# Kernel tuning notes

Hardware: AMD Instinct MI355X
Metric: run time of the kernel (lower is better)

## Reference

```python
import jax, jax.numpy as jnp
import numpy as np

DT = 0.1  # source sets dt = 0.1 globally
B, XS, SS, H = 128, 64, 16, 512  # batch, x_size, s_size, hidden_size


def setup_inputs() -> dict:
    key = jax.random.key(0)
    ks = jax.random.split(key, 14)
    sc = 1.0 / np.sqrt(H)  # PyTorch LSTM/Linear init bound
    u = lambda k, shape: jax.random.uniform(k, shape, jnp.float32, -sc, sc)
    return {
        "x": jax.random.normal(ks[0], (B, XS), jnp.float32),
        "s0": jax.random.normal(ks[1], (B, SS), jnp.float32),
        # LSTM layer 0 (input = x_size + s_size), gate order i,f,g,o
        "W_ih0": u(ks[2], (4 * H, XS + SS)),
        "W_hh0": u(ks[3], (4 * H, H)),
        "b_ih0": u(ks[4], (4 * H,)),
        "b_hh0": u(ks[5], (4 * H,)),
        # LSTM layer 1 (input = hidden)
        "W_ih1": u(ks[6], (4 * H, H)),
        "W_hh1": u(ks[7], (4 * H, H)),
        "b_ih1": u(ks[8], (4 * H,)),
        "b_hh1": u(ks[9], (4 * H,)),
        # fc: hidden -> s_size
        "W_fc": u(ks[10], (SS, H)),
        "b_fc": u(ks[11], (SS,)),
        "max_time": 20,
    }


def _lstm_cell(h, c, inp, W_ih, W_hh, b_ih, b_hh):
    g = inp @ W_ih.T + b_ih + h @ W_hh.T + b_hh  # [B, 4H]
    i, f, gg, o = jnp.split(g, 4, axis=-1)  # torch gate order i,f,g,o
    c = jax.nn.sigmoid(f) * c + jax.nn.sigmoid(i) * jnp.tanh(gg)
    h = jax.nn.sigmoid(o) * jnp.tanh(c)
    return h, c


def reference(x, s0, W_ih0, W_hh0, b_ih0, b_hh0, W_ih1, W_hh1, b_ih1, b_hh1, W_fc, b_fc, max_time):
    T = int(max_time / DT) + 1  # while cal_t <= max_time, cal_t += dt
    batch = x.shape[0]
    hid = W_hh0.shape[1]
    zeros = jnp.zeros((batch, hid), x.dtype)
    init = (zeros, zeros, zeros, zeros, s0)  # (h0,c0,h1,c1,current_s)

    def step(carry, _):
        h0, c0, h1, c1, s = carry
        inp = jnp.concatenate([x, s], axis=-1)  # [B, XS+SS]
        h0, c0 = _lstm_cell(h0, c0, inp, W_ih0, W_hh0, b_ih0, b_hh0)
        h1, c1 = _lstm_cell(h1, c1, h0, W_ih1, W_hh1, b_ih1, b_hh1)
        step_out = h1 @ W_fc.T + b_fc  # [B, SS] (dropout is identity in eval)
        s = s + step_out * DT  # residual Euler update
        return (h0, c0, h1, c1, s), (s, step_out)

    _, (outs, res) = jax.lax.scan(step, init, None, length=T)
    outputs = jnp.transpose(outs, (1, 0, 2))  # [B, T, SS]
    res_steps = jnp.transpose(res, (1, 0, 2))  # [B, T, SS]
    cal_times = jnp.arange(T, dtype=x.dtype) * DT
    return outputs, cal_times, res_steps
```

## Files before the change

### kernel.cpp

```cpp
#include <hip/hip_runtime.h>

#define NB    256
#define BT    1024
#define BATCH 128
#define HID   512
#define XSZ   64
#define SSZ   16
#define CPAD  32
#define SPIN_MAX (1 << 17)

typedef unsigned int uint;
typedef unsigned long long ulong64;
typedef _Float16 half2v __attribute__((ext_vector_type(2)));

#define AL8(p)    __hip_atomic_load((const ulong64*)(p), __ATOMIC_RELAXED, __HIP_MEMORY_SCOPE_AGENT)
#define AS4(p, v) __hip_atomic_store((uint*)(p), (v), __ATOMIC_RELAXED, __HIP_MEMORY_SCOPE_AGENT)

__device__ __align__(16) uint4 g_h0Q[2][64 * 128];
__device__ __align__(16) uint4 g_h1Q[2][64 * 128];
__device__ __align__(16) float g_Wcomb[4 * HID * HID];
__device__ int g_cnt[512 * 8 * CPAD];

__device__ __forceinline__ float sigf(float x) { return 1.f / (1.f + __expf(-x)); }
__device__ __forceinline__ float tanh_fast(float x) {
  float ax = fabsf(x); float e = __expf(-2.f * ax);
  return copysignf((1.f - e) / (1.f + e), x);
}
__device__ __forceinline__ uint pack_f16(float a, float b) {
  half2v h; h.x = (_Float16)a; h.y = (_Float16)b;
  return __builtin_bit_cast(uint, h);
}
__device__ __forceinline__ float2 up2(uint u) {
  half2v h = __builtin_bit_cast(half2v, u);
  return make_float2((float)h.x, (float)h.y);
}
__device__ __forceinline__ float fdot2(uint a, uint w, float c) {
#if __has_builtin(__builtin_amdgcn_fdot2)
  return __builtin_amdgcn_fdot2(__builtin_bit_cast(half2v, a),
                                __builtin_bit_cast(half2v, w), c, false);
#else
  float2 av = up2(a), wv = up2(w);
  return fmaf(av.x, wv.x, fmaf(av.y, wv.y, c));
#endif
}
__device__ __forceinline__ void dot8(uint a, uint4 w0, uint4 w1, float* acc) {
  acc[0] = fdot2(a, w0.x, acc[0]); acc[1] = fdot2(a, w0.y, acc[1]);
  acc[2] = fdot2(a, w0.z, acc[2]); acc[3] = fdot2(a, w0.w, acc[3]);
  acc[4] = fdot2(a, w1.x, acc[4]); acc[5] = fdot2(a, w1.y, acc[5]);
  acc[6] = fdot2(a, w1.z, acc[6]); acc[7] = fdot2(a, w1.w, acc[7]);
}
__device__ __forceinline__ void dots16x2(const uint4* __restrict__ apq,
                                         const uint*  __restrict__ wbA,
                                         const uint*  __restrict__ wbB,
                                         float* __restrict__ accA,
                                         float* __restrict__ accB) {
  const ulong64* ap = (const ulong64*)apq;
  ulong64 lo[16], hi[16];
#pragma unroll
  for (int i = 0; i < 16; ++i) {
    lo[i] = AL8(ap + i * 256);
    hi[i] = AL8(ap + i * 256 + 1);
  }
#pragma unroll
  for (int i = 0; i < 16; ++i) {
    const uint4* wA = (const uint4*)(wbA + 32 * i);
    const uint4* wB = (const uint4*)(wbB + 32 * i);
    uint a0 = (uint)lo[i], a1 = (uint)(lo[i] >> 32);
    uint a2 = (uint)hi[i], a3 = (uint)(hi[i] >> 32);
    dot8(a0, wA[0], wA[1], accA); dot8(a0, wB[0], wB[1], accB);
    dot8(a1, wA[2], wA[3], accA); dot8(a1, wB[2], wB[3], accB);
    dot8(a2, wA[4], wA[5], accA); dot8(a2, wB[4], wB[5], accB);
    dot8(a3, wA[6], wA[7], accA); dot8(a3, wB[6], wB[7], accB);
  }
}

__device__ __forceinline__ void cnt_wait(int pid) {
  const int l = threadIdx.x & 63;
  const int* cp = &g_cnt[(pid * 8 + (l & 7)) * CPAD];
  int guard = 0;
  for (;;) {
    int v = __hip_atomic_load(cp, __ATOMIC_RELAXED, __HIP_MEMORY_SCOPE_AGENT);
    if (__all(v >= 64)) break;
    __builtin_amdgcn_s_sleep(1);
    if (++guard > SPIN_MAX) break;
  }
  __builtin_amdgcn_sched_barrier(0);
}

__device__ __forceinline__ void group_wait(int pid, int pw, int tid, int* rel) {
  if ((tid >> 6) == pw) {
    cnt_wait(pid);
    if ((tid & 63) == 0)
      __hip_atomic_store(&rel[pid & 1], pid, __ATOMIC_RELEASE, __HIP_MEMORY_SCOPE_WORKGROUP);
  } else {
    int guard = 0;
    while (__hip_atomic_load(&rel[pid & 1], __ATOMIC_ACQUIRE, __HIP_MEMORY_SCOPE_WORKGROUP) < pid) {
      __builtin_amdgcn_s_sleep(1);
      if (++guard > SPIN_MAX) break;
    }
    __builtin_amdgcn_sched_barrier(0);
  }
}

__global__ void setup_kernel(float* __restrict__ out, int T) {
  int idx = blockIdx.x * blockDim.x + threadIdx.x;
  int n   = gridDim.x * blockDim.x;
  uint* z0 = (uint*)g_h0Q;
  uint* z1 = (uint*)g_h1Q;
  for (int i = idx; i < 2 * 64 * 128 * 4; i += n) { z0[i] = 0u; z1[i] = 0u; }
  for (int t = idx; t < T; t += n) out[BATCH * T * SSZ + t] = (float)t * 0.1f;
  for (int i = idx; i < 512 * 8 * CPAD; i += n) g_cnt[i] = 0;
}

__global__ void wcomb_kernel(const float* __restrict__ Wih0, const float* __restrict__ Wfc) {
  int idx = blockIdx.x * blockDim.x + threadIdx.x;
  int row = idx >> 9, k = idx & (HID - 1);
  float a = 0.f;
#pragma unroll
  for (int m = 0; m < SSZ; m++) a += Wih0[row * (XSZ + SSZ) + XSZ + m] * Wfc[m * HID + k];
  g_Wcomb[idx] = 0.1f * a;
}

__global__ __launch_bounds__(BT, 4) void persist_kernel(
    const float* __restrict__ x,    const float* __restrict__ s0,
    const float* __restrict__ Wih0, const float* __restrict__ Whh0,
    const float* __restrict__ bih0, const float* __restrict__ bhh0,
    const float* __restrict__ Wih1, const float* __restrict__ Whh1,
    const float* __restrict__ bih1, const float* __restrict__ bhh1,
    const float* __restrict__ Wfc,  const float* __restrict__ bfc,
    float* __restrict__ out, int T)
{
  __shared__ uint  lwT[4][256][8];
  __shared__ float gbuf[8][8][128];
  __shared__ float gbuf1[4][8][128];
  __shared__ float sbase[8][128];
  __shared__ float c0s[2][128], c1s[2][128];
  __shared__ uint  wfcP[16][268];
  __shared__ float b1s[8], ucs[8];
  __shared__ int   rel[2];

  const int bk  = blockIdx.x;
  const int tid = threadIdx.x;
  const int ks  = tid >> 7;
  const int b   = tid & 127;
  const int q0  = (ks & 3) * 16;
  const int kp0 = (ks & 3) * 64;

  if (tid == 0) { rel[0] = -1; rel[1] = -1; }

  for (int e = tid; e < 4 * 256 * 8; e += BT) {
    int mat = e >> 11, kp = (e >> 3) & 255, r = e & 7;
    int row = (r >> 1) * HID + 2 * bk + (r & 1);
    const float* src = (mat == 0) ? &Whh0[row * HID]
                     : (mat == 1) ? &g_Wcomb[row * HID]
                     : (mat == 2) ? &Wih1[row * HID] : &Whh1[row * HID];
    lwT[mat][kp][r] = pack_f16(src[2 * kp], src[2 * kp + 1]);
  }
  for (int e = tid; e < 16 * 256; e += BT) {
    int fs_ = e >> 8, kp = e & 255;
    wfcP[fs_][kp] = pack_f16(Wfc[fs_ * HID + 2 * kp], Wfc[fs_ * HID + 2 * kp + 1]);
  }
  for (int e = tid; e < 4 * 8 * 128; e += BT) ((float*)gbuf)[e] = 0.f;
  {
    int r = tid >> 7, bb = tid & 127;
    int row = (r >> 1) * HID + 2 * bk + (r & 1);
    float a = bih0[row] + bhh0[row];
    const float* wr = Wih0 + row * (XSZ + SSZ);
#pragma unroll 4
    for (int k = 0; k < XSZ; k++) a = fmaf(wr[k], x[bb * XSZ + k], a);
    sbase[r][bb] = a;
  }
  if (tid < 8) {
    int row = (tid >> 1) * HID + 2 * bk + (tid & 1);
    b1s[tid] = bih1[row] + bhh1[row];
    float uc = 0.f;
    const float* ws = Wih0 + row * (XSZ + SSZ) + XSZ;
#pragma unroll
    for (int m = 0; m < SSZ; m++) uc = fmaf(ws[m], bfc[m], uc);
    ucs[tid] = 0.1f * uc;
  }
  __syncthreads();

  float u[8];
  if (tid < 128) {
#pragma unroll
    for (int r = 0; r < 8; r++) {
      int row = (r >> 1) * HID + 2 * bk + (r & 1);
      const float* ws = Wih0 + row * (XSZ + SSZ) + XSZ;
      float a = 0.f;
#pragma unroll
      for (int m = 0; m < SSZ; m++) a = fmaf(ws[m], s0[b * SSZ + m], a);
      u[r] = a - ucs[r];
    }
    c0s[0][b] = 0.f; c0s[1][b] = 0.f;
    c1s[0][b] = 0.f; c1s[1][b] = 0.f;
  }

  const bool fcw = (bk >= 128) && ((tid >> 6) == 15);
  const int  fb = bk - 128, lane = tid & 63, fs = lane & 15, fq = lane >> 4;
  float s_reg = 0.f, bfcj = 0.f;
  if (fcw && lane < SSZ) { s_reg = s0[fb * SSZ + lane]; bfcj = bfc[lane]; }

  auto fc_step = [&](int tt, const uint4* h1base) {
    const ulong64* hp = (const ulong64*)(h1base + fq * 16 * 128 + fb);
    ulong64 lo[16], hi[16];
#pragma unroll
    for (int i = 0; i < 16; ++i) {
      lo[i] = AL8(hp + i * 256);
      hi[i] = AL8(hp + i * 256 + 1);
    }
    const uint4* wp = (const uint4*)&wfcP[fs][fq * 64];
    float acc = 0.f;
#pragma unroll
    for (int i = 0; i < 16; ++i) {
      uint4 w = wp[i];
      acc = fdot2((uint)lo[i],         w.x, acc);
      acc = fdot2((uint)(lo[i] >> 32), w.y, acc);
      acc = fdot2((uint)hi[i],         w.z, acc);
      acc = fdot2((uint)(hi[i] >> 32), w.w, acc);
    }
    acc += __shfl_xor(acc, 16);
    acc += __shfl_xor(acc, 32);
    if (lane < SSZ) {
      float so = acc + bfcj;
      s_reg += 0.1f * so;
      out[fb * (T * SSZ) + tt * SSZ + fs] = s_reg;
      out[BATCH * T * SSZ + T + fb * (T * SSZ) + tt * SSZ + fs] = so;
    }
  };

  int p = 0;
  for (int t = 0; t < T; ++t) {
    if (ks >= 4) {
      if (t > 0) group_wait(2 * t, 8, tid, rel);
      float accA[8] = {0,0,0,0,0,0,0,0}, accB[8] = {0,0,0,0,0,0,0,0};
      dots16x2(g_h1Q[p] + q0 * 128 + b, &lwT[1][kp0][0], &lwT[3][kp0][0], accA, accB);
#pragma unroll
      for (int r = 0; r < 8; r++) { gbuf[ks][r][b] = accA[r]; gbuf1[ks - 4][r][b] = accB[r]; }
    }
    __syncthreads();
    if (tid < 128) {
      float pre[8];
#pragma unroll
      for (int r = 0; r < 8; r++) {
        float s1 = gbuf[0][r][b] + gbuf[1][r][b] + gbuf[2][r][b] + gbuf[3][r][b];
        float s2 = gbuf[4][r][b] + gbuf[5][r][b] + gbuf[6][r][b] + gbuf[7][r][b];
        u[r] += s2 + ucs[r];
        pre[r] = sbase[r][b] + s1 + u[r];
      }
      float h[2];
#pragma unroll
      for (int jj = 0; jj < 2; jj++) {
        float c = c0s[jj][b];
        c = sigf(pre[2 + jj]) * c + sigf(pre[0 + jj]) * tanh_fast(pre[4 + jj]);
        c0s[jj][b] = c;
        h[jj] = sigf(pre[6 + jj]) * tanh_fast(c);
      }
      AS4(((uint*)&g_h0Q[p ^ 1][(bk >> 2) * 128 + b]) + (bk & 3), pack_f16(h[0], h[1]));
      asm volatile("s_waitcnt vmcnt(0)" ::: "memory");
      if ((tid & 63) == 0)
        __hip_atomic_fetch_add(&g_cnt[((2 * t + 1) * 8 + (bk & 7)) * CPAD], 1,
                               __ATOMIC_RELAXED, __HIP_MEMORY_SCOPE_AGENT);
    }
    __syncthreads();
    if (ks < 4) {
      group_wait(2 * t + 1, 0, tid, rel);
      float accA[8] = {0,0,0,0,0,0,0,0}, accB[8] = {0,0,0,0,0,0,0,0};
      dots16x2(g_h0Q[p ^ 1] + q0 * 128 + b, &lwT[2][kp0][0], &lwT[0][kp0][0], accA, accB);
#pragma unroll
      for (int r = 0; r < 8; r++) { gbuf[4 + ks][r][b] = accA[r]; gbuf[ks][r][b] = accB[r]; }
    } else {
      if (fcw && t > 0) fc_step(t - 1, g_h1Q[p]);
    }
    __syncthreads();
    if (tid < 128) {
      float pre[8];
#pragma unroll
      for (int r = 0; r < 8; r++) {
        float s1 = gbuf[4][r][b] + gbuf[5][r][b] + gbuf[6][r][b] + gbuf[7][r][b];
        float s2 = gbuf1[0][r][b] + gbuf1[1][r][b] + gbuf1[2][r][b] + gbuf1[3][r][b];
        pre[r] = b1s[r] + s1 + s2;
      }
      float h[2];
#pragma unroll
      for (int jj = 0; jj < 2; jj++) {
        float c = c1s[jj][b];
        c = sigf(pre[2 + jj]) * c + sigf(pre[0 + jj]) * tanh_fast(pre[4 + jj]);
        c1s[jj][b] = c;
        h[jj] = sigf(pre[6 + jj]) * tanh_fast(c);
      }
      AS4(((uint*)&g_h1Q[p ^ 1][(bk >> 2) * 128 + b]) + (bk & 3), pack_f16(h[0], h[1]));
      asm volatile("s_waitcnt vmcnt(0)" ::: "memory");
      if ((tid & 63) == 0)
        __hip_atomic_fetch_add(&g_cnt[((2 * t + 2) * 8 + (bk & 7)) * CPAD], 1,
                               __ATOMIC_RELAXED, __HIP_MEMORY_SCOPE_AGENT);
    }
    __syncthreads();
    p ^= 1;
  }

  if (fcw) {
    cnt_wait(2 * T);
    fc_step(T - 1, g_h1Q[p]);
  }
}

extern "C" void kernel_launch(void* const* d_in, const int* in_sizes, int n_in,
                              void* d_out, int out_size, void* d_ws, size_t ws_size,
                              hipStream_t stream) {
  const float* x    = (const float*)d_in[0];
  const float* s0   = (const float*)d_in[1];
  const float* Wih0 = (const float*)d_in[2];
  const float* Whh0 = (const float*)d_in[3];
  const float* bih0 = (const float*)d_in[4];
  const float* bhh0 = (const float*)d_in[5];
  const float* Wih1 = (const float*)d_in[6];
  const float* Whh1 = (const float*)d_in[7];
  const float* bih1 = (const float*)d_in[8];
  const float* bhh1 = (const float*)d_in[9];
  const float* Wfc  = (const float*)d_in[10];
  const float* bfc  = (const float*)d_in[11];
  float* out = (float*)d_out;

  const int T = out_size / (2 * BATCH * SSZ + 1);

  setup_kernel<<<64, 256, 0, stream>>>(out, T);
  wcomb_kernel<<<(4 * HID * HID) / 256, 256, 0, stream>>>(Wih0, Wfc);
  persist_kernel<<<NB, BT, 0, stream>>>(x, s0, Wih0, Whh0, bih0, bhh0,
                                        Wih1, Whh1, bih1, bhh1, Wfc, bfc, out, T);
}
```

Baseline: 4.849 ms.

## Spread gate nonlinearity across all threads and use per-quarter arrival counters

The cell update now runs across all 1024 threads, one gate row per thread, with shuffles gathering the i/f/g/o values. Before, only 128 threads did this work, and a block-wide barrier stood between the update and the next matmul. Each block now counts its wavefronts' arrivals in shared memory and bumps one of four global counters, one per quarter of the blocks. Each consumer quarter waits only on the counter for the slice of h it reads, instead of on a broader group wait. This aims to cut the serial elementwise tail and the per-step barrier latency, at the cost of shuffle traffic, spin loops on thread 0, and a larger counter array.

```diff
diff --git a/kernel.cpp b/kernel.cpp
--- a/kernel.cpp
+++ b/kernel.cpp
@@ -19,7 +19,7 @@
 __device__ __align__(16) uint4 g_h0Q[2][64 * 128];
 __device__ __align__(16) uint4 g_h1Q[2][64 * 128];
 __device__ __align__(16) float g_Wcomb[4 * HID * HID];
-__device__ int g_cnt[512 * 8 * CPAD];
+__device__ int g_cnt[2100 * 4 * CPAD];
 
 __device__ __forceinline__ float sigf(float x) { return 1.f / (1.f + __expf(-x)); }
 __device__ __forceinline__ float tanh_fast(float x) {
@@ -49,57 +49,42 @@
   acc[4] = fdot2(a, w1.x, acc[4]); acc[5] = fdot2(a, w1.y, acc[5]);
   acc[6] = fdot2(a, w1.z, acc[6]); acc[7] = fdot2(a, w1.w, acc[7]);
 }
-__device__ __forceinline__ void dots16x2(const uint4* __restrict__ apq,
-                                         const uint*  __restrict__ wbA,
-                                         const uint*  __restrict__ wbB,
-                                         float* __restrict__ accA,
-                                         float* __restrict__ accB) {
+__device__ __forceinline__ void dots_dual(const uint4* __restrict__ apq,
+                                          const uint*  __restrict__ wbA,
+                                          const uint*  __restrict__ wbB,
+                                          float* __restrict__ accA,
+                                          float* __restrict__ accB) {
   const ulong64* ap = (const ulong64*)apq;
-  ulong64 lo[16], hi[16];
-#pragma unroll
-  for (int i = 0; i < 16; ++i) {
-    lo[i] = AL8(ap + i * 256);
-    hi[i] = AL8(ap + i * 256 + 1);
-  }
-#pragma unroll
-  for (int i = 0; i < 16; ++i) {
-    const uint4* wA = (const uint4*)(wbA + 32 * i);
-    const uint4* wB = (const uint4*)(wbB + 32 * i);
-    uint a0 = (uint)lo[i], a1 = (uint)(lo[i] >> 32);
-    uint a2 = (uint)hi[i], a3 = (uint)(hi[i] >> 32);
-    dot8(a0, wA[0], wA[1], accA); dot8(a0, wB[0], wB[1], accB);
-    dot8(a1, wA[2], wA[3], accA); dot8(a1, wB[2], wB[3], accB);
-    dot8(a2, wA[4], wA[5], accA); dot8(a2, wB[4], wB[5], accB);
-    dot8(a3, wA[6], wA[7], accA); dot8(a3, wB[6], wB[7], accB);
-  }
-}
-
-__device__ __forceinline__ void cnt_wait(int pid) {
-  const int l = threadIdx.x & 63;
-  const int* cp = &g_cnt[(pid * 8 + (l & 7)) * CPAD];
+#pragma unroll
+  for (int c = 0; c < 2; ++c) {
+    ulong64 lo[8], hi[8];
+#pragma unroll
+    for (int i = 0; i < 8; ++i) {
+      lo[i] = AL8(ap + (c * 8 + i) * 256);
+      hi[i] = AL8(ap + (c * 8 + i) * 256 + 1);
+    }
+#pragma unroll
+    for (int i = 0; i < 8; ++i) {
+      const uint4* wA = (const uint4*)(wbA + 32 * (c * 8 + i));
+      const uint4* wB = (const uint4*)(wbB + 32 * (c * 8 + i));
+      uint a0 = (uint)lo[i], a1 = (uint)(lo[i] >> 32);
+      uint a2 = (uint)hi[i], a3 = (uint)(hi[i] >> 32);
+      dot8(a0, wA[0], wA[1], accA); dot8(a0, wB[0], wB[1], accB);
+      dot8(a1, wA[2], wA[3], accA); dot8(a1, wB[2], wB[3], accB);
+      dot8(a2, wA[4], wA[5], accA); dot8(a2, wB[4], wB[5], accB);
+      dot8(a3, wA[6], wA[7], accA); dot8(a3, wB[6], wB[7], accB);
+    }
+  }
+}
+
+__device__ __forceinline__ void qwait(int pid, int qtr) {
+  const int* cp = &g_cnt[(pid * 4 + qtr) * CPAD];
   int guard = 0;
-  for (;;) {
-    int v = __hip_atomic_load(cp, __ATOMIC_RELAXED, __HIP_MEMORY_SCOPE_AGENT);
-    if (__all(v >= 64)) break;
+  while (__hip_atomic_load(cp, __ATOMIC_RELAXED, __HIP_MEMORY_SCOPE_AGENT) < NB / 4) {
     __builtin_amdgcn_s_sleep(1);
     if (++guard > SPIN_MAX) break;
   }
   __builtin_amdgcn_sched_barrier(0);
-}
-
-__device__ __forceinline__ void group_wait(int pid, int pw, int tid, int* rel) {
-  if ((tid >> 6) == pw) {
-    cnt_wait(pid);
-    if ((tid & 63) == 0)
-      __hip_atomic_store(&rel[pid & 1], pid, __ATOMIC_RELEASE, __HIP_MEMORY_SCOPE_WORKGROUP);
-  } else {
-    int guard = 0;
-    while (__hip_atomic_load(&rel[pid & 1], __ATOMIC_ACQUIRE, __HIP_MEMORY_SCOPE_WORKGROUP) < pid) {
-      __builtin_amdgcn_s_sleep(1);
-      if (++guard > SPIN_MAX) break;
-    }
-    __builtin_amdgcn_sched_barrier(0);
-  }
 }
 
 __global__ void setup_kernel(float* __restrict__ out, int T) {
@@ -109,7 +94,8 @@
   uint* z1 = (uint*)g_h1Q;
   for (int i = idx; i < 2 * 64 * 128 * 4; i += n) { z0[i] = 0u; z1[i] = 0u; }
   for (int t = idx; t < T; t += n) out[BATCH * T * SSZ + t] = (float)t * 0.1f;
-  for (int i = idx; i < 512 * 8 * CPAD; i += n) g_cnt[i] = 0;
+  int ncnt = (2 * T + 2) * 4 * CPAD;
+  for (int i = idx; i < ncnt; i += n) g_cnt[i] = 0;
 }
 
 __global__ void wcomb_kernel(const float* __restrict__ Wih0, const float* __restrict__ Wfc) {
@@ -131,73 +117,61 @@
     float* __restrict__ out, int T)
 {
   __shared__ uint  lwT[4][256][8];
-  __shared__ float gbuf[8][8][128];
-  __shared__ float gbuf1[4][8][128];
-  __shared__ float sbase[8][128];
-  __shared__ float c0s[2][128], c1s[2][128];
+  __shared__ float gA[4][8][130];
+  __shared__ float gW[4][8][130];
+  __shared__ float gB[8][8][130];
   __shared__ uint  wfcP[16][268];
-  __shared__ float b1s[8], ucs[8];
-  __shared__ int   rel[2];
-
-  const int bk  = blockIdx.x;
-  const int tid = threadIdx.x;
-  const int ks  = tid >> 7;
-  const int b   = tid & 127;
-  const int q0  = (ks & 3) * 16;
-  const int kp0 = (ks & 3) * 64;
-
-  if (tid == 0) { rel[0] = -1; rel[1] = -1; }
+  __shared__ int   arrive;
+
+  const int bk   = blockIdx.x;
+  const int tid  = threadIdx.x;
+  const int ks   = tid >> 7;
+  const int bb   = tid & 127;
+  const int wv   = tid >> 6;
+  const int lane = tid & 63;
+  const int be   = (wv << 3) + (lane >> 3);
+  const int r    = lane & 7;
+  const int myq  = bk >> 6;
+
+  if (tid == 0) arrive = 0;
 
   for (int e = tid; e < 4 * 256 * 8; e += BT) {
-    int mat = e >> 11, kp = (e >> 3) & 255, r = e & 7;
-    int row = (r >> 1) * HID + 2 * bk + (r & 1);
+    int mat = e >> 11, kp = (e >> 3) & 255, rr = e & 7;
+    int row = (rr >> 1) * HID + 2 * bk + (rr & 1);
     const float* src = (mat == 0) ? &Whh0[row * HID]
                      : (mat == 1) ? &g_Wcomb[row * HID]
                      : (mat == 2) ? &Wih1[row * HID] : &Whh1[row * HID];
-    lwT[mat][kp][r] = pack_f16(src[2 * kp], src[2 * kp + 1]);
+    lwT[mat][kp][rr] = pack_f16(src[2 * kp], src[2 * kp + 1]);
   }
   for (int e = tid; e < 16 * 256; e += BT) {
     int fs_ = e >> 8, kp = e & 255;
     wfcP[fs_][kp] = pack_f16(Wfc[fs_ * HID + 2 * kp], Wfc[fs_ * HID + 2 * kp + 1]);
   }
-  for (int e = tid; e < 4 * 8 * 128; e += BT) ((float*)gbuf)[e] = 0.f;
+  for (int e = tid; e < 4 * 8 * 130; e += BT) ((float*)gW)[e] = 0.f;
+
+  const int row_g = (r >> 1) * HID + 2 * bk + (r & 1);
+  float sbase_t = bih0[row_g] + bhh0[row_g];
   {
-    int r = tid >> 7, bb = tid & 127;
-    int row = (r >> 1) * HID + 2 * bk + (r & 1);
-    float a = bih0[row] + bhh0[row];
-    const float* wr = Wih0 + row * (XSZ + SSZ);
+    const float* wr = Wih0 + row_g * (XSZ + SSZ);
 #pragma unroll 4
-    for (int k = 0; k < XSZ; k++) a = fmaf(wr[k], x[bb * XSZ + k], a);
-    sbase[r][bb] = a;
-  }
-  if (tid < 8) {
-    int row = (tid >> 1) * HID + 2 * bk + (tid & 1);
-    b1s[tid] = bih1[row] + bhh1[row];
-    float uc = 0.f;
-    const float* ws = Wih0 + row * (XSZ + SSZ) + XSZ;
-#pragma unroll
-    for (int m = 0; m < SSZ; m++) uc = fmaf(ws[m], bfc[m], uc);
-    ucs[tid] = 0.1f * uc;
-  }
-  __syncthreads();
-
-  float u[8];
-  if (tid < 128) {
-#pragma unroll
-    for (int r = 0; r < 8; r++) {
-      int row = (r >> 1) * HID + 2 * bk + (r & 1);
-      const float* ws = Wih0 + row * (XSZ + SSZ) + XSZ;
-      float a = 0.f;
-#pragma unroll
-      for (int m = 0; m < SSZ; m++) a = fmaf(ws[m], s0[b * SSZ + m], a);
-      u[r] = a - ucs[r];
-    }
-    c0s[0][b] = 0.f; c0s[1][b] = 0.f;
-    c1s[0][b] = 0.f; c1s[1][b] = 0.f;
-  }
-
-  const bool fcw = (bk >= 128) && ((tid >> 6) == 15);
-  const int  fb = bk - 128, lane = tid & 63, fs = lane & 15, fq = lane >> 4;
+    for (int k = 0; k < XSZ; k++) sbase_t = fmaf(wr[k], x[be * XSZ + k], sbase_t);
+  }
+  float ucs_t = 0.f, u_t = 0.f;
+  {
+    const float* ws = Wih0 + row_g * (XSZ + SSZ) + XSZ;
+#pragma unroll
+    for (int m = 0; m < SSZ; m++) {
+      ucs_t = fmaf(ws[m], bfc[m], ucs_t);
+      u_t   = fmaf(ws[m], s0[be * SSZ + m], u_t);
+    }
+    ucs_t *= 0.1f;
+    u_t   -= ucs_t;
+  }
+  const float b1_t = bih1[row_g] + bhh1[row_g];
+  float c0_reg = 0.f, c1_reg = 0.f;
+
+  const bool fcw = (bk >= 128) && (wv == 15);
+  const int  fb = bk - 128, fs = lane & 15, fq = lane >> 4;
   float s_reg = 0.f, bfcj = 0.f;
   if (fcw && lane < SSZ) { s_reg = s0[fb * SSZ + lane]; bfcj = bfc[lane]; }
 
@@ -229,78 +203,98 @@
     }
   };
 
-  int p = 0;
+  __syncthreads();
+
+  int p = 0, ph = 0;
   for (int t = 0; t < T; ++t) {
     if (ks >= 4) {
-      if (t > 0) group_wait(2 * t, 8, tid, rel);
+      if (t > 0) qwait(2 * t, ks & 3);
       float accA[8] = {0,0,0,0,0,0,0,0}, accB[8] = {0,0,0,0,0,0,0,0};
-      dots16x2(g_h1Q[p] + q0 * 128 + b, &lwT[1][kp0][0], &lwT[3][kp0][0], accA, accB);
-#pragma unroll
-      for (int r = 0; r < 8; r++) { gbuf[ks][r][b] = accA[r]; gbuf1[ks - 4][r][b] = accB[r]; }
+      dots_dual(g_h1Q[p] + (ks & 3) * 16 * 128 + bb,
+                &lwT[1][(ks & 3) * 64][0], &lwT[3][(ks & 3) * 64][0], accA, accB);
+#pragma unroll
+      for (int r2 = 0; r2 < 8; r2++) { gA[ks - 4][r2][bb] = accA[r2]; gB[ks][r2][bb] = accB[r2]; }
     }
     __syncthreads();
-    if (tid < 128) {
-      float pre[8];
-#pragma unroll
-      for (int r = 0; r < 8; r++) {
-        float s1 = gbuf[0][r][b] + gbuf[1][r][b] + gbuf[2][r][b] + gbuf[3][r][b];
-        float s2 = gbuf[4][r][b] + gbuf[5][r][b] + gbuf[6][r][b] + gbuf[7][r][b];
-        u[r] += s2 + ucs[r];
-        pre[r] = sbase[r][b] + s1 + u[r];
+    {
+      float s1 = gW[0][r][be] + gW[1][r][be] + gW[2][r][be] + gW[3][r][be];
+      float s2 = gA[0][r][be] + gA[1][r][be] + gA[2][r][be] + gA[3][r][be];
+      u_t += s2 + ucs_t;
+      float pre = sbase_t + s1 + u_t;
+      float pf = __shfl_xor(pre, 2);
+      float pg = __shfl_xor(pre, 4);
+      float po = __shfl_xor(pre, 6);
+      float c = sigf(pf) * c0_reg + sigf(pre) * tanh_fast(pg);
+      if (r < 2) c0_reg = c;
+      float h = sigf(po) * tanh_fast(c);
+      float hx = __shfl_xor(h, 1);
+      if (r == 0)
+        AS4(((uint*)&g_h0Q[p ^ 1][(bk >> 2) * 128 + be]) + (bk & 3), pack_f16(h, hx));
+      asm volatile("s_waitcnt vmcnt(0)" ::: "memory");
+      if (lane == 0)
+        __hip_atomic_fetch_add(&arrive, 1, __ATOMIC_RELEASE, __HIP_MEMORY_SCOPE_WORKGROUP);
+      ++ph;
+      if (tid == 0) {
+        int g2 = 0;
+        while (__hip_atomic_load(&arrive, __ATOMIC_ACQUIRE, __HIP_MEMORY_SCOPE_WORKGROUP) < 16 * ph) {
+          __builtin_amdgcn_s_sleep(0);
+          if (++g2 > SPIN_MAX) break;
+        }
+        __hip_atomic_fetch_add(&g_cnt[((2 * t + 1) * 4 + myq) * CPAD], 1,
+                               __ATOMIC_RELAXED, __HIP_MEMORY_SCOPE_AGENT);
       }
-      float h[2];
-#pragma unroll
-      for (int jj = 0; jj < 2; jj++) {
-        float c = c0s[jj][b];
-        c = sigf(pre[2 + jj]) * c + sigf(pre[0 + jj]) * tanh_fast(pre[4 + jj]);
-        c0s[jj][b] = c;
-        h[jj] = sigf(pre[6 + jj]) * tanh_fast(c);
-      }
-      AS4(((uint*)&g_h0Q[p ^ 1][(bk >> 2) * 128 + b]) + (bk & 3), pack_f16(h[0], h[1]));
-      asm volatile("s_waitcnt vmcnt(0)" ::: "memory");
-      if ((tid & 63) == 0)
-        __hip_atomic_fetch_add(&g_cnt[((2 * t + 1) * 8 + (bk & 7)) * CPAD], 1,
-                               __ATOMIC_RELAXED, __HIP_MEMORY_SCOPE_AGENT);
-    }
-    __syncthreads();
+    }
     if (ks < 4) {
-      group_wait(2 * t + 1, 0, tid, rel);
+      qwait(2 * t + 1, ks);
       float accA[8] = {0,0,0,0,0,0,0,0}, accB[8] = {0,0,0,0,0,0,0,0};
-      dots16x2(g_h0Q[p ^ 1] + q0 * 128 + b, &lwT[2][kp0][0], &lwT[0][kp0][0], accA, accB);
-#pragma unroll
-      for (int r = 0; r < 8; r++) { gbuf[4 + ks][r][b] = accA[r]; gbuf[ks][r][b] = accB[r]; }
+      dots_dual(g_h0Q[p ^ 1] + ks * 16 * 128 + bb,
+                &lwT[2][ks * 64][0], &lwT[0][ks * 64][0], accA, accB);
+#pragma unroll
+      for (int r2 = 0; r2 < 8; r2++) { gB[ks][r2][bb] = accA[r2]; gW[ks][r2][bb] = accB[r2]; }
     } else {
       if (fcw && t > 0) fc_step(t - 1, g_h1Q[p]);
     }
     __syncthreads();
-    if (tid < 128) {
-      float pre[8];
-#pragma unroll
-      for (int r = 0; r < 8; r++) {
-        float s1 = gbuf[4][r][b] + gbuf[5][r][b] + gbuf[6][r][b] + gbuf[7][r][b];
-        float s2 = gbuf1[0][r][b] + gbuf1[1][r][b] + gbuf1[2][r][b] + gbuf1[3][r][b];
-        pre[r] = b1s[r] + s1 + s2;
+    {
+      float s1 = gB[0][r][be] + gB[1][r][be] + gB[2][r][be] + gB[3][r][be];
+      float s2 = gB[4][r][be] + gB[5][r][be] + gB[6][r][be] + gB[7][r][be];
+      float pre = b1_t + s1 + s2;
+      float pf = __shfl_xor(pre, 2);
+      float pg = __shfl_xor(pre, 4);
+      float po = __shfl_xor(pre, 6);
+      float c = sigf(pf) * c1_reg + sigf(pre) * tanh_fast(pg);
+      if (r < 2) c1_reg = c;
+      float h = sigf(po) * tanh_fast(c);
+      float hx = __shfl_xor(h, 1);
+      if (r == 0)
+        AS4(((uint*)&g_h1Q[p ^ 1][(bk >> 2) * 128 + be]) + (bk & 3), pack_f16(h, hx));
+      asm volatile("s_waitcnt vmcnt(0)" ::: "memory");
+      if (lane == 0)
+        __hip_atomic_fetch_add(&arrive, 1, __ATOMIC_RELEASE, __HIP_MEMORY_SCOPE_WORKGROUP);
+      ++ph;
+      if (tid == 0) {
+        int g2 = 0;
+        while (__hip_atomic_load(&arrive, __ATOMIC_ACQUIRE, __HIP_MEMORY_SCOPE_WORKGROUP) < 16 * ph) {
+          __builtin_amdgcn_s_sleep(0);
+          if (++g2 > SPIN_MAX) break;
+        }
+        __hip_atomic_fetch_add(&g_cnt[((2 * t + 2) * 4 + myq) * CPAD], 1,
+                               __ATOMIC_RELAXED, __HIP_MEMORY_SCOPE_AGENT);
       }
-      float h[2];
-#pragma unroll
-      for (int jj = 0; jj < 2; jj++) {
-        float c = c1s[jj][b];
-        c = sigf(pre[2 + jj]) * c + sigf(pre[0 + jj]) * tanh_fast(pre[4 + jj]);
-        c1s[jj][b] = c;
-        h[jj] = sigf(pre[6 + jj]) * tanh_fast(c);
+    }
+    p ^= 1;
+  }
+
+  if (fcw) {
+    for (int q = 0; q < 4; ++q) {
+      int guard = 0;
+      while (__hip_atomic_load(&g_cnt[(2 * T * 4 + q) * CPAD],
+                               __ATOMIC_RELAXED, __HIP_MEMORY_SCOPE_AGENT) < NB / 4) {
+        __builtin_amdgcn_s_sleep(2);
+        if (++guard > SPIN_MAX) break;
       }
-      AS4(((uint*)&g_h1Q[p ^ 1][(bk >> 2) * 128 + b]) + (bk & 3), pack_f16(h[0], h[1]));
-      asm volatile("s_waitcnt vmcnt(0)" ::: "memory");
-      if ((tid & 63) == 0)
-        __hip_atomic_fetch_add(&g_cnt[((2 * t + 2) * 8 + (bk & 7)) * CPAD], 1,
-                               __ATOMIC_RELAXED, __HIP_MEMORY_SCOPE_AGENT);
-    }
-    __syncthreads();
-    p ^= 1;
-  }
-
-  if (fcw) {
-    cnt_wait(2 * T);
+    }
+    __builtin_amdgcn_sched_barrier(0);
     fc_step(T - 1, g_h1Q[p]);
   }
 }
```

New measurement: 6.411 ms. +32.2%, slower.
